# Performance work log

Hardware: AMD Instinct MI355X
Metric: run time of the kernel (lower is better)

## Reference

```python
import jax, jax.numpy as jnp
import numpy as np

D_IN = 1024
D_OUT = 1024
NUM_HEADS = 16
HEAD_DIM = D_OUT // NUM_HEADS


def setup_inputs() -> dict:
    key = jax.random.key(0)
    kx, kq, kk, kv, ko = jax.random.split(key, 5)
    s = 1.0 / np.sqrt(D_IN)
    return {
        "x": jax.random.normal(kx, (1, 4096, D_IN), dtype=jnp.float32),
        "Wq": jax.random.normal(kq, (D_IN, D_OUT), dtype=jnp.float32) * s,
        "Wk": jax.random.normal(kk, (D_IN, D_OUT), dtype=jnp.float32) * s,
        "Wv": jax.random.normal(kv, (D_IN, D_OUT), dtype=jnp.float32) * s,
        "Wo": jax.random.normal(ko, (D_OUT, D_OUT), dtype=jnp.float32) * s,
    }


def reference(x, Wq, Wk, Wv, Wo):
    b, s, _ = x.shape
    # project and split heads: [b, h, s, d]
    def split_heads(t):
        return t.reshape(b, s, NUM_HEADS, HEAD_DIM).transpose(0, 2, 1, 3)
    Q = split_heads(x @ Wq)
    K = split_heads(x @ Wk)
    V = split_heads(x @ Wv)
    scores = jnp.einsum("bhqd,bhkd->bhqk", Q, K) / jnp.sqrt(jnp.float32(HEAD_DIM))
    causal = jnp.triu(jnp.ones((s, s), dtype=bool), k=1)  # True above diagonal
    scores = jnp.where(causal, -jnp.inf, scores)
    probs = jax.nn.softmax(scores, axis=-1)
    out = jnp.einsum("bhqk,bhkd->bhqd", probs, V)
    out = out.transpose(0, 2, 1, 3).reshape(b, s, D_OUT)
    return out @ Wo
```

## Files before the change

### kernel.cpp

```cpp
#include <hip/hip_runtime.h>
#include <cstdint>

#define S_LEN 4096
#define D_MODEL 1024
#define NHEAD 16
#define HDIM 64

typedef __bf16 bf16_t;
typedef __bf16 bf16x8 __attribute__((ext_vector_type(8)));
typedef __bf16 bf16x4 __attribute__((ext_vector_type(4)));
typedef float floatx4 __attribute__((ext_vector_type(4)));

#define QSCALE 0.18033688011112042f
#define NCHUNK_Q 160

__device__ __forceinline__ void lds_cp16(void* lds, const void* g) {
    __builtin_amdgcn_global_load_lds(
        (const __attribute__((address_space(1))) unsigned int*)g,
        (__attribute__((address_space(3))) unsigned int*)lds,
        16, 0, 0);
}

__device__ __forceinline__ float fast_exp2(float x) {
    float r;
    asm("v_exp_f32 %0, %1" : "=v"(r) : "v"(x));
    return r;
}

__global__ __launch_bounds__(256) void k_prep(const float* __restrict__ x,
                                              const float* __restrict__ Wq,
                                              const float* __restrict__ Wk,
                                              const float* __restrict__ Wv,
                                              const float* __restrict__ Wo,
                                              bf16_t* __restrict__ xb,
                                              bf16_t* __restrict__ WtQKV,
                                              bf16_t* __restrict__ WtO,
                                              unsigned int* __restrict__ ctr) {
    const int bx = blockIdx.x;
    if (bx < 4096) {
        int i = bx * 256 + threadIdx.x;
        float4 v = ((const float4*)x)[i];
        bf16x4 o;
        o[0] = (bf16_t)v.x; o[1] = (bf16_t)v.y; o[2] = (bf16_t)v.z; o[3] = (bf16_t)v.w;
        *(bf16x4*)(xb + (size_t)i * 4) = o;
        return;
    }
    if (bx == 4096 && threadIdx.x < 8) ctr[threadIdx.x * 16] = 0u;
    __shared__ float lds[64][65];
    const int i = bx - 4096;
    const int z = i >> 8, rem = i & 255;
    const float* W = (z == 0) ? Wq : (z == 1) ? Wk : (z == 2) ? Wv : Wo;
    bf16_t* Wt = (z < 3) ? (WtQKV + (size_t)z * 1048576) : WtO;
    const int k0 = (rem >> 4) * 64, n0 = (rem & 15) * 64;
    const int t = threadIdx.x, cl = t & 63, rl = t >> 6;
#pragma unroll
    for (int r = 0; r < 16; ++r)
        lds[r * 4 + rl][cl] = W[(size_t)(k0 + r * 4 + rl) * 1024 + n0 + cl];
    __syncthreads();
#pragma unroll
    for (int r = 0; r < 16; ++r)
        Wt[(size_t)(n0 + r * 4 + rl) * 1024 + k0 + cl] = (bf16_t)lds[cl][r * 4 + rl];
}

template <int MODE, int MT>
__global__ __launch_bounds__(256) void k_gemm(const bf16_t* __restrict__ A,
                                              const bf16_t* __restrict__ Bt,
                                              float* __restrict__ Cout,
                                              bf16_t* __restrict__ Qb,
                                              bf16_t* __restrict__ Kb,
                                              bf16_t* __restrict__ Vt,
                                              const bf16_t* __restrict__ OP1x,
                                              const bf16_t* __restrict__ OP2x,
                                              const float* __restrict__ Lpx) {
    constexpr int MI = MT / 32;
    __shared__ __align__(16) bf16_t sA[MT * 32];
    __shared__ __align__(16) bf16_t sB[128 * 32];
    const int t = threadIdx.x, w = t >> 6, lane = t & 63, quad = lane >> 4, l15 = lane & 15;
    const int m0 = blockIdx.x * MT, n0 = blockIdx.y * 128;
    const int wm = w >> 1, wn = w & 1;

    floatx4 acc[MI][4];
#pragma unroll
    for (int i = 0; i < MI; ++i)
#pragma unroll
        for (int j = 0; j < 4; ++j)
            acc[i][j] = floatx4{0.f, 0.f, 0.f, 0.f};

    const int crow = m0 + (t >> 2), ckq = t & 3;
    const bool hasC = (MODE == 2) && (crow >= 2048);
    bf16x8 cA{}, cB{}, cC{};
    float cla = 0.f, clb = 0.f, clc = 0.f;
    if (MODE == 2) {
        cA = *(const bf16x8*)(A + (size_t)crow * 1024 + ckq * 8);
        cB = *(const bf16x8*)(OP1x + (size_t)crow * 1024 + ckq * 8);
        cla = Lpx[crow];
        clb = Lpx[65536 + crow];
        if (hasC) {
            cC = *(const bf16x8*)(OP2x + (size_t)(crow - 2048) * 1024 + ckq * 8);
            clc = Lpx[131072 + crow];
        }
    }

    for (int kb = 0; kb < 32; ++kb) {
        __syncthreads();
        if (MODE == 2) {
            float inv = __builtin_amdgcn_rcpf(cla + clb + clc);
            bf16x8 o;
#pragma unroll
            for (int e = 0; e < 8; ++e)
                o[e] = (bf16_t)(((float)cA[e] + (float)cB[e] + (float)cC[e]) * inv);
            *(bf16x8*)&sA[t * 8] = o;
            if (kb + 1 < 32) {
                int h2 = (kb + 1) >> 1;
                int col = (kb + 1) * 32 + ckq * 8;
                cA = *(const bf16x8*)(A + (size_t)crow * 1024 + col);
                cB = *(const bf16x8*)(OP1x + (size_t)crow * 1024 + col);
                cla = Lpx[h2 * 4096 + crow];
                clb = Lpx[65536 + h2 * 4096 + crow];
                if (hasC) {
                    cC = *(const bf16x8*)(OP2x + (size_t)(crow - 2048) * 1024 + col);
                    clc = Lpx[131072 + h2 * 4096 + crow];
                }
            }
        } else {
#pragma unroll
            for (int r = 0; r < MT / 64; ++r) {
                int c = t + 256 * r;
                int row = c >> 2, kq = c & 3;
                lds_cp16(&sA[w * 512 + r * 2048],
                         A + (size_t)(m0 + row) * 1024 + kb * 32 + kq * 8);
            }
        }
#pragma unroll
        for (int r = 0; r < 2; ++r) {
            int c = t + 256 * r;
            int row = c >> 2, kq = c & 3;
            lds_cp16(&sB[w * 512 + r * 2048],
                     Bt + (size_t)(n0 + row) * 1024 + kb * 32 + kq * 8);
        }
        __syncthreads();
        bf16x8 af[MI], bfr[4];
#pragma unroll
        for (int i = 0; i < MI; ++i)
            af[i] = *(const bf16x8*)&sA[(wm * (MT / 2) + i * 16 + l15) * 32 + quad * 8];
#pragma unroll
        for (int j = 0; j < 4; ++j)
            bfr[j] = *(const bf16x8*)&sB[(wn * 64 + j * 16 + l15) * 32 + quad * 8];
#pragma unroll
        for (int i = 0; i < MI; ++i)
#pragma unroll
            for (int j = 0; j < 4; ++j)
                acc[i][j] = __builtin_amdgcn_mfma_f32_16x16x32_bf16(af[i], bfr[j],
                                                                    acc[i][j], 0, 0, 0);
    }

    const int mrow = m0 + wm * (MT / 2) + quad * 4;
    if (MODE == 0 || MODE == 2) {
        const int ncol = n0 + wn * 64 + l15;
#pragma unroll
        for (int i = 0; i < MI; ++i)
#pragma unroll
            for (int j = 0; j < 4; ++j)
#pragma unroll
                for (int r = 0; r < 4; ++r)
                    Cout[(size_t)(mrow + i * 16 + r) * 1024 + ncol + j * 16] = acc[i][j][r];
    } else {
        const int g = (int)blockIdx.y >> 3;
        const int ncbase = ((int)blockIdx.y & 7) * 128 + wn * 64 + l15;
        if (g == 2) {
#pragma unroll
            for (int j = 0; j < 4; ++j) {
                int nc = ncbase + j * 16;
                int hh = nc >> 6, dd = nc & 63;
                bf16_t* dst = Vt + (size_t)hh * 262144 + (size_t)dd * 64;
#pragma unroll
                for (int i = 0; i < MI; ++i) {
                    int s0r = mrow + i * 16;
                    bf16x4 pk;
                    pk[0] = (bf16_t)acc[i][j][0]; pk[1] = (bf16_t)acc[i][j][1];
                    pk[2] = (bf16_t)acc[i][j][2]; pk[3] = (bf16_t)acc[i][j][3];
                    int kk = s0r & 63;
                    int pp = (kk & 0x20) | ((kk & 0xC) << 1) | ((kk & 0x10) >> 2);
                    *(bf16x4*)&dst[(size_t)(s0r >> 6) * 4096 + pp] = pk;
                }
            }
        } else {
            bf16_t* base = g ? Kb : Qb;
            const float sc = g ? 1.0f : QSCALE;
#pragma unroll
            for (int j = 0; j < 4; ++j) {
                int nc = ncbase + j * 16;
                int hh = nc >> 6, dd = nc & 63;
#pragma unroll
                for (int i = 0; i < MI; ++i)
#pragma unroll
                    for (int r = 0; r < 4; ++r)
                        base[(size_t)hh * 262144 + (size_t)(mrow + i * 16 + r) * 64 + dd] =
                            (bf16_t)(acc[i][j][r] * sc);
            }
        }
    }
}

__global__ __launch_bounds__(256, 4) void k_attn(const bf16_t* __restrict__ Qb,
                                                 const bf16_t* __restrict__ Kb,
                                                 const bf16_t* __restrict__ Vt,
                                                 bf16_t* __restrict__ OP0,
                                                 bf16_t* __restrict__ OP1,
                                                 bf16_t* __restrict__ OP2,
                                                 float* __restrict__ Lp,
                                                 unsigned int* __restrict__ ctr) {
    __shared__ __align__(16) bf16_t Ks[2][64 * 64];
    __shared__ __align__(16) bf16_t Vts[2][64 * 64];
    __shared__ int sid;
    const int t = threadIdx.x, w = t >> 6, quad = (t & 63) >> 4, l15 = t & 15;
    const int q8 = (int)blockIdx.x & 7;
    unsigned int* qctr = ctr + q8 * 16;

    bf16x8 vones;
#pragma unroll
    for (int e = 0; e < 8; ++e) vones[e] = (bf16_t)1.0f;

#define STAGE_K(b, kb_)                                                            \
    {                                                                              \
        _Pragma("unroll") for (int r = 0; r < 2; ++r) {                            \
            int c = t + 256 * r;                                                   \
            int row = c >> 3, sw = (c & 7) ^ (row & 7);                            \
            lds_cp16(&Ks[b][c * 8], Kh + (size_t)(kb_) * 4096 + row * 64 + sw * 8);\
        }                                                                          \
    }
#define STAGE_V(b, kb_)                                                            \
    {                                                                              \
        _Pragma("unroll") for (int r = 0; r < 2; ++r) {                            \
            int c = t + 256 * r;                                                   \
            int row = c >> 3, sw = (c & 7) ^ (row & 7);                            \
            lds_cp16(&Vts[b][c * 8], Vth + (size_t)(kb_) * 4096 + row * 64 + sw * 8);\
        }                                                                          \
    }

    for (;;) {
        if (t == 0) sid = (int)atomicAdd(qctr, 1u);
        __syncthreads();
        const int u = sid;
        if (u >= NCHUNK_Q) break;

        int qb, hh, part, c0, c1;
        if (u < 96) {
            qb = 31 - u / 6;
            int r = u % 6;
            hh = r & 1; part = r >> 1;
            int L = 2 * qb + 2, base = L / 3, rem = L % 3;
            int mn = part < rem ? part : rem;
            c0 = part * base + mn;
            c1 = c0 + base + (part < rem ? 1 : 0);
        } else {
            int v = u - 96;
            qb = 15 - (v >> 2);
            int r = v & 3;
            hh = r & 1; part = r >> 1;
            c0 = part ? (qb + 1) : 0;
            c1 = part ? (2 * qb + 2) : (qb + 1);
        }
        const int h = q8 * 2 + hh;
        const bf16_t* Qh = Qb + (size_t)h * 262144;
        const bf16_t* Kh = Kb + (size_t)h * 262144;
        const bf16_t* Vth = Vt + (size_t)h * 262144;

        const bf16_t* Qrow = Qh + (size_t)(qb * 128 + w * 32 + l15) * 64;
        bf16x8 bq[2][2];
#pragma unroll
        for (int qt = 0; qt < 2; ++qt)
#pragma unroll
            for (int kh = 0; kh < 2; ++kh)
                bq[qt][kh] = *(const bf16x8*)(Qrow + qt * 1024 + kh * 32 + quad * 8);

        floatx4 lacc[2];
        floatx4 o_acc[2][4];
#pragma unroll
        for (int qt = 0; qt < 2; ++qt) {
            lacc[qt] = floatx4{0.f, 0.f, 0.f, 0.f};
#pragma unroll
            for (int j = 0; j < 4; ++j) o_acc[qt][j] = floatx4{0.f, 0.f, 0.f, 0.f};
        }

        const int nIter = c1 - c0;
        const int qmax = qb * 128 + w * 32 + 31;

        STAGE_K(0, c0)
        STAGE_V(0, c0)
        for (int it = 0; it < nIter; ++it) {
            const int kb = c0 + it;
            const int buf = it & 1;
            __syncthreads();
            if (it + 1 < nIter) {
                STAGE_K(buf ^ 1, kb + 1)
                STAGE_V(buf ^ 1, kb + 1)
            }
            const bool active = (kb * 64 <= qmax);

            if (active) {
                floatx4 st[2][4];
                __builtin_amdgcn_s_setprio(1);
#pragma unroll
                for (int j = 0; j < 4; ++j) {
                    int rk = j * 16 + l15;
                    bf16x8 a0 = *(const bf16x8*)&Ks[buf][rk * 64 + ((quad ^ (rk & 7)) * 8)];
                    bf16x8 a1 = *(const bf16x8*)&Ks[buf][rk * 64 + (((quad + 4) ^ (rk & 7)) * 8)];
#pragma unroll
                    for (int qt = 0; qt < 2; ++qt) {
                        floatx4 z = {0.f, 0.f, 0.f, 0.f};
                        st[qt][j] = __builtin_amdgcn_mfma_f32_16x16x32_bf16(a0, bq[qt][0], z, 0, 0, 0);
                        st[qt][j] = __builtin_amdgcn_mfma_f32_16x16x32_bf16(a1, bq[qt][1], st[qt][j], 0, 0, 0);
                    }
                }
                __builtin_amdgcn_s_setprio(0);
                if (kb >= 2 * qb) {
#pragma unroll
                    for (int qt = 0; qt < 2; ++qt) {
                        int qg = qb * 128 + w * 32 + qt * 16 + l15;
#pragma unroll
                        for (int j = 0; j < 4; ++j)
#pragma unroll
                            for (int r = 0; r < 4; ++r) {
                                int keyg = kb * 64 + j * 16 + quad * 4 + r;
                                if (keyg > qg) st[qt][j][r] = -1e30f;
                            }
                    }
                }
                bf16x8 pa[2][2];
#pragma unroll
                for (int qt = 0; qt < 2; ++qt) {
#pragma unroll
                    for (int j = 0; j < 4; ++j) {
                        st[qt][j][0] = fast_exp2(st[qt][j][0]);
                        st[qt][j][1] = fast_exp2(st[qt][j][1]);
                        st[qt][j][2] = fast_exp2(st[qt][j][2]);
                        st[qt][j][3] = fast_exp2(st[qt][j][3]);
                    }
#pragma unroll
                    for (int kh = 0; kh < 2; ++kh)
#pragma unroll
                        for (int m = 0; m < 4; ++m) {
                            pa[qt][kh][m]     = (bf16_t)st[qt][2 * kh][m];
                            pa[qt][kh][4 + m] = (bf16_t)st[qt][2 * kh + 1][m];
                        }
                }
                __builtin_amdgcn_s_setprio(1);
#pragma unroll
                for (int kh = 0; kh < 2; ++kh) {
                    int pc = kh * 4 + quad;
#pragma unroll
                    for (int j = 0; j < 4; ++j) {
                        int rd = j * 16 + l15;
                        bf16x8 bv = *(const bf16x8*)&Vts[buf][rd * 64 + ((pc ^ (rd & 7)) * 8)];
                        o_acc[0][j] = __builtin_amdgcn_mfma_f32_16x16x32_bf16(pa[0][kh], bv, o_acc[0][j], 0, 0, 0);
                        o_acc[1][j] = __builtin_amdgcn_mfma_f32_16x16x32_bf16(pa[1][kh], bv, o_acc[1][j], 0, 0, 0);
                    }
                    lacc[0] = __builtin_amdgcn_mfma_f32_16x16x32_bf16(pa[0][kh], vones, lacc[0], 0, 0, 0);
                    lacc[1] = __builtin_amdgcn_mfma_f32_16x16x32_bf16(pa[1][kh], vones, lacc[1], 0, 0, 0);
                }
                __builtin_amdgcn_s_setprio(0);
            }
        }
        bf16_t* OPx = (part == 0) ? OP0 : (part == 1) ? OP1 : OP2;
        const int rsub = (part == 2) ? 2048 : 0;
#pragma unroll
        for (int qt = 0; qt < 2; ++qt) {
            if (l15 == 0)
                *(floatx4*)&Lp[part * 65536 + h * 4096 + qb * 128 + w * 32 + qt * 16 + quad * 4] =
                    lacc[qt];
#pragma unroll
            for (int r = 0; r < 4; ++r) {
                int rowg = qb * 128 + w * 32 + qt * 16 + quad * 4 + r;
#pragma unroll
                for (int j = 0; j < 4; ++j)
                    OPx[(size_t)(rowg - rsub) * 1024 + h * 64 + j * 16 + l15] =
                        (bf16_t)o_acc[qt][j][r];
            }
        }
    }
#undef STAGE_K
#undef STAGE_V
}

extern "C" void kernel_launch(void* const* d_in, const int* in_sizes, int n_in,
                              void* d_out, int out_size, void* d_ws, size_t ws_size,
                              hipStream_t stream) {
    const float* x  = (const float*)d_in[0];
    const float* Wq = (const float*)d_in[1];
    const float* Wk = (const float*)d_in[2];
    const float* Wv = (const float*)d_in[3];
    const float* Wo = (const float*)d_in[4];

    bf16_t* ws = (bf16_t*)d_ws;
    bf16_t* Xb    = ws;
    bf16_t* WtQKV = Xb + 4194304;
    bf16_t* WtO   = WtQKV + 3145728;
    bf16_t* Qb    = WtO + 1048576;
    bf16_t* Kb    = Qb + 4194304;
    bf16_t* Vt    = Kb + 4194304;
    bf16_t* OP1   = Vt + 4194304;
    bf16_t* OP0   = Xb;
    float*  Lp    = (float*)WtQKV;
    bf16_t* OP2   = WtQKV + 393216;
    float* out = (float*)d_out;
    unsigned int* ctr = (unsigned int*)d_out;

    k_prep<<<5120, 256, 0, stream>>>(x, Wq, Wk, Wv, Wo, Xb, WtQKV, WtO, ctr);
    k_gemm<1, 128><<<dim3(32, 24), 256, 0, stream>>>(Xb, WtQKV, nullptr, Qb, Kb, Vt,
                                                     nullptr, nullptr, nullptr);
    k_attn<<<1024, 256, 0, stream>>>(Qb, Kb, Vt, OP0, OP1, OP2, Lp, ctr);
    k_gemm<2, 64><<<dim3(64, 8), 256, 0, stream>>>(OP0, WtO, out, nullptr, nullptr,
                                                   nullptr, OP1, OP2, Lp);
}
```

Measured before the change: 189.2 us.

## Software-pipeline QK^T of next key block with softmax/PV of previous block

Restructures the attention inner loop so that the QK^T MFMAs for key block i run in the same step as exp and PV for block i-1, using two ping-ponged score register sets unrolled by two. K and V staging are split around the compute, and __syncthreads is replaced with explicit vmcnt waits plus s_barrier. The aim is to overlap the exp and convert VALU work with matrix instructions and to hide LDS and global-to-LDS load latency. In exchange it uses more registers, which may lower occupancy, and the hand-written vmcnt counts risk races if the load accounting is wrong.

New measurement: 409.7 us. 116% more time.

```diff
diff --git a/kernel.cpp b/kernel.cpp
--- a/kernel.cpp
+++ b/kernel.cpp
@@ -238,6 +238,73 @@
         }                                                                          \
     }
 
+#define QK_STEP(ST, KBUF, KB)                                                       \
+    if ((KB) * 64 <= qmax) {                                                        \
+        __builtin_amdgcn_s_setprio(1);                                              \
+        _Pragma("unroll") for (int j = 0; j < 4; ++j) {                             \
+            int rk = j * 16 + l15;                                                  \
+            bf16x8 a0 = *(const bf16x8*)&Ks[KBUF][rk * 64 + ((quad ^ (rk & 7)) * 8)]; \
+            bf16x8 a1 = *(const bf16x8*)&Ks[KBUF][rk * 64 + (((quad + 4) ^ (rk & 7)) * 8)]; \
+            _Pragma("unroll") for (int qt = 0; qt < 2; ++qt) {                      \
+                floatx4 z = {0.f, 0.f, 0.f, 0.f};                                   \
+                ST[qt][j] = __builtin_amdgcn_mfma_f32_16x16x32_bf16(a0, bq[qt][0], z, 0, 0, 0); \
+                ST[qt][j] = __builtin_amdgcn_mfma_f32_16x16x32_bf16(a1, bq[qt][1], ST[qt][j], 0, 0, 0); \
+            }                                                                       \
+        }                                                                           \
+        __builtin_amdgcn_s_setprio(0);                                              \
+        if ((KB) >= 2 * qb) {                                                       \
+            _Pragma("unroll") for (int qt = 0; qt < 2; ++qt) {                      \
+                int qg = qb * 128 + w * 32 + qt * 16 + l15;                         \
+                _Pragma("unroll") for (int j = 0; j < 4; ++j)                       \
+                    _Pragma("unroll") for (int r = 0; r < 4; ++r) {                 \
+                        int keyg = (KB) * 64 + j * 16 + quad * 4 + r;               \
+                        if (keyg > qg) ST[qt][j][r] = -1e30f;                       \
+                    }                                                               \
+            }                                                                       \
+        }                                                                           \
+    }
+
+#define SM_PV(ST, KB, VBUF)                                                         \
+    if ((KB) * 64 <= qmax) {                                                        \
+        bf16x8 pa[2][2];                                                            \
+        _Pragma("unroll") for (int qt = 0; qt < 2; ++qt) {                          \
+            _Pragma("unroll") for (int j = 0; j < 4; ++j) {                         \
+                ST[qt][j][0] = fast_exp2(ST[qt][j][0]);                             \
+                ST[qt][j][1] = fast_exp2(ST[qt][j][1]);                             \
+                ST[qt][j][2] = fast_exp2(ST[qt][j][2]);                             \
+                ST[qt][j][3] = fast_exp2(ST[qt][j][3]);                             \
+            }                                                                       \
+            _Pragma("unroll") for (int kh = 0; kh < 2; ++kh)                        \
+                _Pragma("unroll") for (int m = 0; m < 4; ++m) {                     \
+                    pa[qt][kh][m]     = (bf16_t)ST[qt][2 * kh][m];                  \
+                    pa[qt][kh][4 + m] = (bf16_t)ST[qt][2 * kh + 1][m];              \
+                }                                                                   \
+        }                                                                           \
+        __builtin_amdgcn_s_setprio(1);                                              \
+        _Pragma("unroll") for (int kh = 0; kh < 2; ++kh) {                          \
+            int pc = kh * 4 + quad;                                                 \
+            _Pragma("unroll") for (int j = 0; j < 4; ++j) {                         \
+                int rd = j * 16 + l15;                                              \
+                bf16x8 bv = *(const bf16x8*)&Vts[VBUF][rd * 64 + ((pc ^ (rd & 7)) * 8)]; \
+                o_acc[0][j] = __builtin_amdgcn_mfma_f32_16x16x32_bf16(pa[0][kh], bv, o_acc[0][j], 0, 0, 0); \
+                o_acc[1][j] = __builtin_amdgcn_mfma_f32_16x16x32_bf16(pa[1][kh], bv, o_acc[1][j], 0, 0, 0); \
+            }                                                                       \
+            lacc[0] = __builtin_amdgcn_mfma_f32_16x16x32_bf16(pa[0][kh], vones, lacc[0], 0, 0, 0); \
+            lacc[1] = __builtin_amdgcn_mfma_f32_16x16x32_bf16(pa[1][kh], vones, lacc[1], 0, 0, 0); \
+        }                                                                           \
+        __builtin_amdgcn_s_setprio(0);                                              \
+    }
+
+#define ITER(STC, STP, IT)                                                          \
+    {                                                                               \
+        asm volatile("s_waitcnt vmcnt(2)" ::: "memory");                            \
+        __builtin_amdgcn_s_barrier();                                               \
+        if ((IT) + 1 < nIter) STAGE_K(((IT) + 1) & 1, c0 + (IT) + 1)                \
+        QK_STEP(STC, (IT) & 1, c0 + (IT))                                           \
+        SM_PV(STP, c0 + (IT) - 1, ((IT) - 1) & 1)                                   \
+        if ((IT) + 1 < nIter) STAGE_V(((IT) + 1) & 1, c0 + (IT) + 1)                \
+    }
+
     for (;;) {
         if (t == 0) sid = (int)atomicAdd(qctr, 1u);
         __syncthreads();
@@ -285,83 +352,32 @@
 
         const int nIter = c1 - c0;
         const int qmax = qb * 128 + w * 32 + 31;
+        floatx4 stA[2][4], stB[2][4];
 
         STAGE_K(0, c0)
         STAGE_V(0, c0)
-        for (int it = 0; it < nIter; ++it) {
-            const int kb = c0 + it;
-            const int buf = it & 1;
-            __syncthreads();
-            if (it + 1 < nIter) {
-                STAGE_K(buf ^ 1, kb + 1)
-                STAGE_V(buf ^ 1, kb + 1)
-            }
-            const bool active = (kb * 64 <= qmax);
-
-            if (active) {
-                floatx4 st[2][4];
-                __builtin_amdgcn_s_setprio(1);
-#pragma unroll
-                for (int j = 0; j < 4; ++j) {
-                    int rk = j * 16 + l15;
-                    bf16x8 a0 = *(const bf16x8*)&Ks[buf][rk * 64 + ((quad ^ (rk & 7)) * 8)];
-                    bf16x8 a1 = *(const bf16x8*)&Ks[buf][rk * 64 + (((quad + 4) ^ (rk & 7)) * 8)];
-#pragma unroll
-                    for (int qt = 0; qt < 2; ++qt) {
-                        floatx4 z = {0.f, 0.f, 0.f, 0.f};
-                        st[qt][j] = __builtin_amdgcn_mfma_f32_16x16x32_bf16(a0, bq[qt][0], z, 0, 0, 0);
-                        st[qt][j] = __builtin_amdgcn_mfma_f32_16x16x32_bf16(a1, bq[qt][1], st[qt][j], 0, 0, 0);
-                    }
-                }
-                __builtin_amdgcn_s_setprio(0);
-                if (kb >= 2 * qb) {
-#pragma unroll
-                    for (int qt = 0; qt < 2; ++qt) {
-                        int qg = qb * 128 + w * 32 + qt * 16 + l15;
-#pragma unroll
-                        for (int j = 0; j < 4; ++j)
-#pragma unroll
-                            for (int r = 0; r < 4; ++r) {
-                                int keyg = kb * 64 + j * 16 + quad * 4 + r;
-                                if (keyg > qg) st[qt][j][r] = -1e30f;
-                            }
-                    }
-                }
-                bf16x8 pa[2][2];
-#pragma unroll
-                for (int qt = 0; qt < 2; ++qt) {
-#pragma unroll
-                    for (int j = 0; j < 4; ++j) {
-                        st[qt][j][0] = fast_exp2(st[qt][j][0]);
-                        st[qt][j][1] = fast_exp2(st[qt][j][1]);
-                        st[qt][j][2] = fast_exp2(st[qt][j][2]);
-                        st[qt][j][3] = fast_exp2(st[qt][j][3]);
-                    }
-#pragma unroll
-                    for (int kh = 0; kh < 2; ++kh)
-#pragma unroll
-                        for (int m = 0; m < 4; ++m) {
-                            pa[qt][kh][m]     = (bf16_t)st[qt][2 * kh][m];
-                            pa[qt][kh][4 + m] = (bf16_t)st[qt][2 * kh + 1][m];
-                        }
-                }
-                __builtin_amdgcn_s_setprio(1);
-#pragma unroll
-                for (int kh = 0; kh < 2; ++kh) {
-                    int pc = kh * 4 + quad;
-#pragma unroll
-                    for (int j = 0; j < 4; ++j) {
-                        int rd = j * 16 + l15;
-                        bf16x8 bv = *(const bf16x8*)&Vts[buf][rd * 64 + ((pc ^ (rd & 7)) * 8)];
-                        o_acc[0][j] = __builtin_amdgcn_mfma_f32_16x16x32_bf16(pa[0][kh], bv, o_acc[0][j], 0, 0, 0);
-                        o_acc[1][j] = __builtin_amdgcn_mfma_f32_16x16x32_bf16(pa[1][kh], bv, o_acc[1][j], 0, 0, 0);
-                    }
-                    lacc[0] = __builtin_amdgcn_mfma_f32_16x16x32_bf16(pa[0][kh], vones, lacc[0], 0, 0, 0);
-                    lacc[1] = __builtin_amdgcn_mfma_f32_16x16x32_bf16(pa[1][kh], vones, lacc[1], 0, 0, 0);
-                }
-                __builtin_amdgcn_s_setprio(0);
-            }
-        }
+        asm volatile("s_waitcnt vmcnt(2)" ::: "memory");
+        __builtin_amdgcn_s_barrier();
+        if (nIter > 1) STAGE_K(1, c0 + 1)
+        QK_STEP(stA, 0, c0)
+        if (nIter > 1) STAGE_V(1, c0 + 1)
+
+        int it = 1;
+        for (; it + 1 < nIter; it += 2) {
+            ITER(stB, stA, it)
+            ITER(stA, stB, it + 1)
+        }
+        if (it < nIter) {
+            ITER(stB, stA, it)
+            asm volatile("s_waitcnt vmcnt(0)" ::: "memory");
+            __builtin_amdgcn_s_barrier();
+            SM_PV(stB, c0 + nIter - 1, (nIter - 1) & 1)
+        } else {
+            asm volatile("s_waitcnt vmcnt(0)" ::: "memory");
+            __builtin_amdgcn_s_barrier();
+            SM_PV(stA, c0 + nIter - 1, (nIter - 1) & 1)
+        }
+
         bf16_t* OPx = (part == 0) ? OP0 : (part == 1) ? OP1 : OP2;
         const int rsub = (part == 2) ? 2048 : 0;
 #pragma unroll
@@ -379,6 +395,9 @@
             }
         }
     }
+#undef ITER
+#undef SM_PV
+#undef QK_STEP
 #undef STAGE_K
 #undef STAGE_V
 }
```
